# Kernel tuning notes

Hardware: AMD Instinct MI355X
Metric: run time of the kernel (lower is better)

## Reference

```python
import jax, jax.numpy as jnp
import numpy as np

NUM_HEADS = 16
HEAD_DIM = 64  # dim_qkv // num_heads


def setup_inputs() -> dict:
    key = jax.random.key(0)
    ks = jax.random.split(key, 6)
    B, N, D = 2, 2048, 1024
    s = 1.0 / np.sqrt(D)
    x = jax.random.normal(ks[0], (B, N, D), dtype=jnp.float32)
    Wq = jax.random.normal(ks[1], (D, D), dtype=jnp.float32) * s
    Wk = jax.random.normal(ks[2], (D, D), dtype=jnp.float32) * s
    Wv = jax.random.normal(ks[3], (D, D), dtype=jnp.float32) * s
    Wo = jax.random.normal(ks[4], (D, D), dtype=jnp.float32) * s
    z = jnp.zeros((D,), dtype=jnp.float32)
    return {"x": x, "Wq": Wq, "bq": z, "Wk": Wk, "bk": z,
            "Wv": Wv, "bv": z, "Wo": Wo, "bo": z}


def _split_heads(t):
    # [B, N, H*dh] -> [B, H, N, dh]
    B, N, _ = t.shape
    return t.reshape(B, N, NUM_HEADS, HEAD_DIM).transpose(0, 2, 1, 3)


def reference(x, Wq, bq, Wk, bk, Wv, bv, Wo, bo):
    q = _split_heads(x @ Wq + bq)
    k = _split_heads(x @ Wk + bk)
    v = _split_heads(x @ Wv + bv)
    scores = jnp.einsum('bhnd,bhmd->bhnm', q, k) / jnp.sqrt(
        jnp.asarray(HEAD_DIM, dtype=x.dtype))
    attn = jax.nn.softmax(scores, axis=-1)
    heads = jnp.einsum('bhnm,bhmd->bhnd', attn, v)  # [B, H, N, dh]
    B, H, N, dh = heads.shape
    merged = heads.transpose(0, 2, 1, 3).reshape(B, N, H * dh)
    # dropout is identity in deterministic/eval mode
    return merged @ Wo + bo
```

## Files before the change

### kernel.cpp

```cpp
#include <hip/hip_runtime.h>
#include <hip/hip_bf16.h>

typedef __bf16 bf16;
typedef __attribute__((ext_vector_type(8))) __bf16 bf16x8;
typedef __attribute__((ext_vector_type(4))) __bf16 bf16x4;
typedef __attribute__((ext_vector_type(4))) float f32x4;
typedef __attribute__((ext_vector_type(16))) float f32x16;
typedef unsigned int uint;

#define MFMA16(a, b, c) __builtin_amdgcn_mfma_f32_16x16x32_bf16(a, b, c, 0, 0, 0)
#define MFMA32(a, b, c) __builtin_amdgcn_mfma_f32_32x32x16_bf16(a, b, c, 0, 0, 0)

#define GLOAD_LDS(gp, lp) \
  __builtin_amdgcn_global_load_lds( \
      (const __attribute__((address_space(1))) void*)(gp), \
      (__attribute__((address_space(3))) void*)(lp), 16, 0, 0)

#define QSCALE 0.18033688011112042f

__device__ __forceinline__ uint pack2(float a, float b) {
  unsigned short x = __builtin_bit_cast(unsigned short, (bf16)a);
  unsigned short y = __builtin_bit_cast(unsigned short, (bf16)b);
  return (uint)x | ((uint)y << 16);
}

__global__ __launch_bounds__(256) void cvt_x_kernel(const float* __restrict__ x,
                                                    bf16* __restrict__ y) {
  int i = (blockIdx.x * 256 + threadIdx.x) * 8;
  float4 a = *(const float4*)(x + i);
  float4 b = *(const float4*)(x + i + 4);
  bf16x8 v;
  v[0] = (bf16)a.x; v[1] = (bf16)a.y; v[2] = (bf16)a.z; v[3] = (bf16)a.w;
  v[4] = (bf16)b.x; v[5] = (bf16)b.y; v[6] = (bf16)b.z; v[7] = (bf16)b.w;
  *(bf16x8*)(y + i) = v;
}

__global__ __launch_bounds__(256) void wtrans_kernel(
    const float* __restrict__ W0, const float* __restrict__ W1,
    const float* __restrict__ W2, const float* __restrict__ W3,
    bf16* __restrict__ T0, bf16* __restrict__ T1,
    bf16* __restrict__ T2, bf16* __restrict__ T3) {
  const float* W; bf16* T;
  switch (blockIdx.z) {
    case 0: W = W0; T = T0; break;
    case 1: W = W1; T = T1; break;
    case 2: W = W2; T = T2; break;
    default: W = W3; T = T3; break;
  }
  const float scl = (blockIdx.z == 0) ? QSCALE : 1.0f;
  __shared__ float tile[32][33];
  int tx = threadIdx.x & 31;
  int ty = threadIdx.x >> 5;
  int bx = blockIdx.x * 32, by = blockIdx.y * 32;
#pragma unroll
  for (int i = 0; i < 32; i += 8)
    tile[ty + i][tx] = W[(size_t)(by + ty + i) * 1024 + bx + tx];
  __syncthreads();
#pragma unroll
  for (int i = 0; i < 32; i += 8)
    T[(size_t)(bx + ty + i) * 1024 + by + tx] = (bf16)(tile[tx][ty + i] * scl);
}

template <int MODE>
__global__ __launch_bounds__(256, 2) void gemm_kernel(
    const bf16* __restrict__ A, const bf16* __restrict__ Bt,
    const float* __restrict__ b0, const float* __restrict__ b1,
    const float* __restrict__ b2, bf16* __restrict__ o0,
    bf16* __restrict__ o1, bf16* __restrict__ o2, float* __restrict__ of) {
  __shared__ bf16 As[128 * 64];
  __shared__ bf16 Bs[128 * 64];
  const int t = threadIdx.x;
  const int lane = t & 63, wid = t >> 6;
  const int wy = wid >> 1, wx = wid & 1;
  const int lr = lane & 15, lg = lane >> 4;
  const int bm = blockIdx.y, bn = blockIdx.x;
  const bf16* Arow = A + (size_t)bm * 128 * 1024;
  const bf16* Brow = Bt + (size_t)bn * 128 * 1024;
  f32x4 acc[4][4] = {};

  for (int k0 = 0; k0 < 1024; k0 += 64) {
    __syncthreads();
#pragma unroll
    for (int i = 0; i < 4; i++) {
      int off = i * 256 + t;
      int row = off >> 3, ch = off & 7;
      int gch = ch ^ (row & 7);
      GLOAD_LDS(Arow + (size_t)row * 1024 + k0 + gch * 8, As + off * 8);
    }
#pragma unroll
    for (int i = 0; i < 4; i++) {
      int off = i * 256 + t;
      int row = off >> 3, ch = off & 7;
      int gch = ch ^ (row & 7);
      GLOAD_LDS(Brow + (size_t)row * 1024 + k0 + gch * 8, Bs + off * 8);
    }
    __syncthreads();
#pragma unroll
    for (int kh = 0; kh < 2; kh++) {
      bf16x8 af[4], bfr[4];
#pragma unroll
      for (int i = 0; i < 4; i++) {
        int row = wy * 64 + i * 16 + lr;
        int c = kh * 4 + lg;
        af[i] = *(const bf16x8*)(As + row * 64 + ((c ^ (row & 7)) << 3));
      }
#pragma unroll
      for (int j = 0; j < 4; j++) {
        int row = wx * 64 + j * 16 + lr;
        int c = kh * 4 + lg;
        bfr[j] = *(const bf16x8*)(Bs + row * 64 + ((c ^ (row & 7)) << 3));
      }
#pragma unroll
      for (int i = 0; i < 4; i++)
#pragma unroll
        for (int j = 0; j < 4; j++)
          acc[i][j] = MFMA16(af[i], bfr[j], acc[i][j]);
    }
  }

  const int seg = (MODE == 0) ? (bn >> 3) : 0;
  const float* bias = (MODE == 1) ? b0 : (seg == 0 ? b0 : (seg == 1 ? b1 : b2));
  const float bscale = (MODE == 0 && seg == 0) ? QSCALE : 1.0f;

#pragma unroll
  for (int i = 0; i < 4; i++) {
    const int rowb = bm * 128 + wy * 64 + i * 16 + lg * 4;
#pragma unroll
    for (int j = 0; j < 4; j++) {
      const int np = bn * 128 + wx * 64 + j * 16 + lr;
      const int col = np & 1023;
      const float bv = bias[col] * bscale;
      if (MODE == 1) {
#pragma unroll
        for (int r = 0; r < 4; r++)
          of[(size_t)(rowb + r) * 1024 + np] = acc[i][j][r] + bv;
      } else {
        const int h = col >> 6, d = col & 63;
        const int bb = rowb >> 11, nn = rowb & 2047;
        if (seg == 2) {
          bf16x4 pk;
#pragma unroll
          for (int r = 0; r < 4; r++) pk[r] = (bf16)(acc[i][j][r] + bv);
          *(bf16x4*)(o2 + (((size_t)bb * 16 + h) * 64 + d) * 2048 + nn) = pk;
        } else {
          bf16* dst = (seg == 0) ? o0 : o1;
#pragma unroll
          for (int r = 0; r < 4; r++)
            dst[(((size_t)bb * 16 + h) * 2048 + nn + r) * 64 + d] =
                (bf16)(acc[i][j][r] + bv);
        }
      }
    }
  }
}

__global__ __launch_bounds__(256, 2) void attn_kernel(
    const bf16* __restrict__ Q, const bf16* __restrict__ K,
    const bf16* __restrict__ Vt, bf16* __restrict__ Mg) {
  __shared__ bf16 Kl[2][4096];
  __shared__ bf16 Vl[2][4096];
  const int t = threadIdx.x;
  const int lane = t & 63, w = t >> 6;
  const int l31 = lane & 31, hi = lane >> 5;
  const int bh = blockIdx.y;
  const int b = bh >> 4, h = bh & 15;
  const bf16* Qh = Q + (size_t)bh * 2048 * 64;
  const bf16* Kh = K + (size_t)bh * 2048 * 64;
  const bf16* Vh = Vt + (size_t)bh * 64 * 2048;
  const int q_row = blockIdx.x * 128 + w * 32 + l31;

  bf16x8 qf[4];
#pragma unroll
  for (int dblk = 0; dblk < 4; dblk++)
    qf[dblk] = *(const bf16x8*)(Qh + (size_t)q_row * 64 + dblk * 16 + hi * 8);

  f32x16 o0 = {}, o1 = {};
  float lrun = 0.f;

#define STAGE(kt_, buf_)                                                     \
  {                                                                          \
    _Pragma("unroll") for (int i = 0; i < 2; i++) {                          \
      int off = i * 256 + t;                                                 \
      int row = off >> 3, ch = off & 7;                                      \
      int gch = ch ^ (row & 7);                                              \
      GLOAD_LDS(Kh + (size_t)(kt_) * 4096 + row * 64 + gch * 8,              \
                &Kl[buf_][off * 8]);                                         \
      GLOAD_LDS(Vh + (size_t)row * 2048 + (kt_) * 64 + gch * 8,              \
                &Vl[buf_][off * 8]);                                         \
    }                                                                        \
  }

  STAGE(0, 0);
  __syncthreads();

  for (int kt = 0; kt < 32; kt++) {
    const int cur = kt & 1;
    if (kt < 31) STAGE(kt + 1, cur ^ 1);

    f32x16 s0 = {}, s1 = {};
#pragma unroll
    for (int dblk = 0; dblk < 4; dblk++) {
      int c = dblk * 2 + hi;
      bf16x8 kf0 = *(const bf16x8*)&Kl[cur][l31 * 64 + ((c ^ (l31 & 7)) << 3)];
      bf16x8 kf1 = *(const bf16x8*)&Kl[cur][(32 + l31) * 64 + ((c ^ (l31 & 7)) << 3)];
      s0 = MFMA32(kf0, qf[dblk], s0);
      s1 = MFMA32(kf1, qf[dblk], s1);
    }

    float rs = 0.f;
#pragma unroll
    for (int r = 0; r < 16; r++) {
      s0[r] = __builtin_amdgcn_exp2f(s0[r]);
      s1[r] = __builtin_amdgcn_exp2f(s1[r]);
      rs += s0[r] + s1[r];
    }
    rs += __shfl_xor(rs, 32);
    lrun += rs;

    uint prc[8], prd[8];
#pragma unroll
    for (int s = 0; s < 4; s++) {
      prc[s] = pack2(s0[4 * s + 0], s0[4 * s + 1]);
      prd[s] = pack2(s0[4 * s + 2], s0[4 * s + 3]);
      prc[4 + s] = pack2(s1[4 * s + 0], s1[4 * s + 1]);
      prd[4 + s] = pack2(s1[4 * s + 2], s1[4 * s + 3]);
    }

#pragma unroll
    for (int kb = 0; kb < 4; kb++) {
      const int sb = (kb >> 1) * 4 + (kb & 1) * 2;
      uint sendc = hi ? prc[sb] : prc[sb + 1];
      uint sendd = hi ? prd[sb] : prd[sb + 1];
      uint recvc = __shfl_xor(sendc, 32);
      uint recvd = __shfl_xor(sendd, 32);
      union { uint u[4]; bf16x8 v; } pf;
      pf.u[0] = hi ? recvc : prc[sb];
      pf.u[1] = hi ? recvd : prd[sb];
      pf.u[2] = hi ? prc[sb + 1] : recvc;
      pf.u[3] = hi ? prd[sb + 1] : recvd;

      int c = kb * 2 + hi;
      bf16x8 vt0 = *(const bf16x8*)&Vl[cur][l31 * 64 + ((c ^ (l31 & 7)) << 3)];
      bf16x8 vt1 = *(const bf16x8*)&Vl[cur][(32 + l31) * 64 + ((c ^ (l31 & 7)) << 3)];
      o0 = MFMA32(vt0, pf.v, o0);
      o1 = MFMA32(vt1, pf.v, o1);
    }

    __syncthreads();
  }

  const float inv = 1.f / lrun;
  bf16* orow = Mg + ((size_t)b * 2048 + q_row) * 1024 + h * 64;
#pragma unroll
  for (int s = 0; s < 4; s++) {
    bf16x4 p0, p1;
#pragma unroll
    for (int r = 0; r < 4; r++) {
      p0[r] = (bf16)(o0[4 * s + r] * inv);
      p1[r] = (bf16)(o1[4 * s + r] * inv);
    }
    *(bf16x4*)(orow + s * 8 + hi * 4) = p0;
    *(bf16x4*)(orow + 32 + s * 8 + hi * 4) = p1;
  }
}

extern "C" void kernel_launch(void* const* d_in, const int* in_sizes, int n_in,
                              void* d_out, int out_size, void* d_ws, size_t ws_size,
                              hipStream_t stream) {
  const float* x  = (const float*)d_in[0];
  const float* Wq = (const float*)d_in[1];
  const float* bq = (const float*)d_in[2];
  const float* Wk = (const float*)d_in[3];
  const float* bk = (const float*)d_in[4];
  const float* Wv = (const float*)d_in[5];
  const float* bv = (const float*)d_in[6];
  const float* Wo = (const float*)d_in[7];
  const float* bo = (const float*)d_in[8];
  float* out = (float*)d_out;
  char* ws = (char*)d_ws;
  const size_t MiB = 1u << 20;

  bf16* Xb    = (bf16*)(ws);
  bf16* Mg    = Xb;
  bf16* Wqkv  = (bf16*)(ws + 8 * MiB);
  bf16* WoT   = (bf16*)(ws + 14 * MiB);
  bf16* Qb    = (bf16*)(ws + 16 * MiB);
  bf16* Kb    = (bf16*)(ws + 24 * MiB);
  bf16* Vtb   = (bf16*)(ws + 32 * MiB);

  cvt_x_kernel<<<2048, 256, 0, stream>>>(x, Xb);
  wtrans_kernel<<<dim3(32, 32, 4), 256, 0, stream>>>(
      Wq, Wk, Wv, Wo, Wqkv, Wqkv + (1u << 20), Wqkv + (2u << 20), WoT);
  gemm_kernel<0><<<dim3(24, 32), 256, 0, stream>>>(
      Xb, Wqkv, bq, bk, bv, Qb, Kb, Vtb, nullptr);
  attn_kernel<<<dim3(16, 32), 256, 0, stream>>>(Qb, Kb, Vtb, Mg);
  gemm_kernel<1><<<dim3(8, 32), 256, 0, stream>>>(
      Mg, WoT, bo, nullptr, nullptr, nullptr, nullptr, nullptr, out);
  (void)in_sizes; (void)n_in; (void)out_size; (void)ws_size;
}
```

Before: 129.9 us.

## Merge prep kernels, XCD-aware block remap, larger attention K/V tiles, narrower output GEMM tiles

The x conversion and weight transpose kernels are merged into one launch, saving a kernel launch. The QKV GEMM, output GEMM and attention now remap block indices so that neighbouring tiles (or all query blocks of one head) land on the same XCD for L2 reuse. Attention stages 128-key tiles instead of 64, halving the loop iterations and barriers at the cost of doubled LDS use and more registers. The output projection becomes a dedicated kernel with 128x64 tiles, doubling the grid to improve CU occupancy.

```diff
diff --git a/kernel.cpp b/kernel.cpp
--- a/kernel.cpp
+++ b/kernel.cpp
@@ -24,34 +24,37 @@
   return (uint)x | ((uint)y << 16);
 }
 
-__global__ __launch_bounds__(256) void cvt_x_kernel(const float* __restrict__ x,
-                                                    bf16* __restrict__ y) {
-  int i = (blockIdx.x * 256 + threadIdx.x) * 8;
-  float4 a = *(const float4*)(x + i);
-  float4 b = *(const float4*)(x + i + 4);
-  bf16x8 v;
-  v[0] = (bf16)a.x; v[1] = (bf16)a.y; v[2] = (bf16)a.z; v[3] = (bf16)a.w;
-  v[4] = (bf16)b.x; v[5] = (bf16)b.y; v[6] = (bf16)b.z; v[7] = (bf16)b.w;
-  *(bf16x8*)(y + i) = v;
-}
-
-__global__ __launch_bounds__(256) void wtrans_kernel(
+__global__ __launch_bounds__(256) void prep_kernel(
+    const float* __restrict__ x, bf16* __restrict__ y,
     const float* __restrict__ W0, const float* __restrict__ W1,
     const float* __restrict__ W2, const float* __restrict__ W3,
     bf16* __restrict__ T0, bf16* __restrict__ T1,
     bf16* __restrict__ T2, bf16* __restrict__ T3) {
+  const int bid = blockIdx.x;
+  if (bid < 2048) {
+    int i = (bid * 256 + threadIdx.x) * 8;
+    float4 a = *(const float4*)(x + i);
+    float4 b = *(const float4*)(x + i + 4);
+    bf16x8 v;
+    v[0] = (bf16)a.x; v[1] = (bf16)a.y; v[2] = (bf16)a.z; v[3] = (bf16)a.w;
+    v[4] = (bf16)b.x; v[5] = (bf16)b.y; v[6] = (bf16)b.z; v[7] = (bf16)b.w;
+    *(bf16x8*)(y + i) = v;
+    return;
+  }
+  const int wq = bid - 2048;
+  const int z = wq >> 10, rem = wq & 1023;
   const float* W; bf16* T;
-  switch (blockIdx.z) {
+  switch (z) {
     case 0: W = W0; T = T0; break;
     case 1: W = W1; T = T1; break;
     case 2: W = W2; T = T2; break;
     default: W = W3; T = T3; break;
   }
-  const float scl = (blockIdx.z == 0) ? QSCALE : 1.0f;
+  const float scl = (z == 0) ? QSCALE : 1.0f;
   __shared__ float tile[32][33];
   int tx = threadIdx.x & 31;
   int ty = threadIdx.x >> 5;
-  int bx = blockIdx.x * 32, by = blockIdx.y * 32;
+  int bx = (rem & 31) * 32, by = (rem >> 5) * 32;
 #pragma unroll
   for (int i = 0; i < 32; i += 8)
     tile[ty + i][tx] = W[(size_t)(by + ty + i) * 1024 + bx + tx];
@@ -61,19 +64,20 @@
     T[(size_t)(bx + ty + i) * 1024 + by + tx] = (bf16)(tile[tx][ty + i] * scl);
 }
 
-template <int MODE>
-__global__ __launch_bounds__(256, 2) void gemm_kernel(
+__global__ __launch_bounds__(256, 2) void gemm_qkv_kernel(
     const bf16* __restrict__ A, const bf16* __restrict__ Bt,
     const float* __restrict__ b0, const float* __restrict__ b1,
     const float* __restrict__ b2, bf16* __restrict__ o0,
-    bf16* __restrict__ o1, bf16* __restrict__ o2, float* __restrict__ of) {
+    bf16* __restrict__ o1, bf16* __restrict__ o2) {
   __shared__ bf16 As[128 * 64];
   __shared__ bf16 Bs[128 * 64];
+  const int f = blockIdx.y * 24 + blockIdx.x;
+  const int wg = (f % 8) * 96 + f / 8;
+  const int bn = wg % 24, bm = wg / 24;
   const int t = threadIdx.x;
   const int lane = t & 63, wid = t >> 6;
   const int wy = wid >> 1, wx = wid & 1;
   const int lr = lane & 15, lg = lane >> 4;
-  const int bm = blockIdx.y, bn = blockIdx.x;
   const bf16* Arow = A + (size_t)bm * 128 * 1024;
   const bf16* Brow = Bt + (size_t)bn * 128 * 1024;
   f32x4 acc[4][4] = {};
@@ -118,9 +122,9 @@
     }
   }
 
-  const int seg = (MODE == 0) ? (bn >> 3) : 0;
-  const float* bias = (MODE == 1) ? b0 : (seg == 0 ? b0 : (seg == 1 ? b1 : b2));
-  const float bscale = (MODE == 0 && seg == 0) ? QSCALE : 1.0f;
+  const int seg = bn >> 3;
+  const float* bias = (seg == 0) ? b0 : (seg == 1 ? b1 : b2);
+  const float bscale = (seg == 0) ? QSCALE : 1.0f;
 
 #pragma unroll
   for (int i = 0; i < 4; i++) {
@@ -130,26 +134,90 @@
       const int np = bn * 128 + wx * 64 + j * 16 + lr;
       const int col = np & 1023;
       const float bv = bias[col] * bscale;
-      if (MODE == 1) {
+      const int h = col >> 6, d = col & 63;
+      const int bb = rowb >> 11, nn = rowb & 2047;
+      if (seg == 2) {
+        bf16x4 pk;
+#pragma unroll
+        for (int r = 0; r < 4; r++) pk[r] = (bf16)(acc[i][j][r] + bv);
+        *(bf16x4*)(o2 + (((size_t)bb * 16 + h) * 64 + d) * 2048 + nn) = pk;
+      } else {
+        bf16* dst = (seg == 0) ? o0 : o1;
 #pragma unroll
         for (int r = 0; r < 4; r++)
-          of[(size_t)(rowb + r) * 1024 + np] = acc[i][j][r] + bv;
-      } else {
-        const int h = col >> 6, d = col & 63;
-        const int bb = rowb >> 11, nn = rowb & 2047;
-        if (seg == 2) {
-          bf16x4 pk;
-#pragma unroll
-          for (int r = 0; r < 4; r++) pk[r] = (bf16)(acc[i][j][r] + bv);
-          *(bf16x4*)(o2 + (((size_t)bb * 16 + h) * 64 + d) * 2048 + nn) = pk;
-        } else {
-          bf16* dst = (seg == 0) ? o0 : o1;
-#pragma unroll
-          for (int r = 0; r < 4; r++)
-            dst[(((size_t)bb * 16 + h) * 2048 + nn + r) * 64 + d] =
-                (bf16)(acc[i][j][r] + bv);
-        }
-      }
+          dst[(((size_t)bb * 16 + h) * 2048 + nn + r) * 64 + d] =
+              (bf16)(acc[i][j][r] + bv);
+      }
+    }
+  }
+}
+
+__global__ __launch_bounds__(256, 2) void gemmo_kernel(
+    const bf16* __restrict__ A, const bf16* __restrict__ Bt,
+    const float* __restrict__ bias, float* __restrict__ out) {
+  __shared__ bf16 As[128 * 64];
+  __shared__ bf16 Bs[64 * 64];
+  const int f = blockIdx.y * 16 + blockIdx.x;
+  const int wg = (f & 7) * 64 + (f >> 3);
+  const int bn = wg & 15, bm = wg >> 4;
+  const int t = threadIdx.x;
+  const int lane = t & 63, wid = t >> 6;
+  const int wy = wid >> 1, wx = wid & 1;
+  const int lr = lane & 15, lg = lane >> 4;
+  const bf16* Arow = A + (size_t)bm * 128 * 1024;
+  const bf16* Brow = Bt + (size_t)bn * 64 * 1024;
+  f32x4 acc[4][2] = {};
+
+  for (int k0 = 0; k0 < 1024; k0 += 64) {
+    __syncthreads();
+#pragma unroll
+    for (int i = 0; i < 4; i++) {
+      int off = i * 256 + t;
+      int row = off >> 3, ch = off & 7;
+      int gch = ch ^ (row & 7);
+      GLOAD_LDS(Arow + (size_t)row * 1024 + k0 + gch * 8, As + off * 8);
+    }
+#pragma unroll
+    for (int i = 0; i < 2; i++) {
+      int off = i * 256 + t;
+      int row = off >> 3, ch = off & 7;
+      int gch = ch ^ (row & 7);
+      GLOAD_LDS(Brow + (size_t)row * 1024 + k0 + gch * 8, Bs + off * 8);
+    }
+    __syncthreads();
+#pragma unroll
+    for (int kh = 0; kh < 2; kh++) {
+      bf16x8 af[4], bfr[2];
+#pragma unroll
+      for (int i = 0; i < 4; i++) {
+        int row = wy * 64 + i * 16 + lr;
+        int c = kh * 4 + lg;
+        af[i] = *(const bf16x8*)(As + row * 64 + ((c ^ (row & 7)) << 3));
+      }
+#pragma unroll
+      for (int j = 0; j < 2; j++) {
+        int row = wx * 32 + j * 16 + lr;
+        int c = kh * 4 + lg;
+        bfr[j] = *(const bf16x8*)(Bs + row * 64 + ((c ^ (row & 7)) << 3));
+      }
+#pragma unroll
+      for (int i = 0; i < 4; i++)
+#pragma unroll
+        for (int j = 0; j < 2; j++)
+          acc[i][j] = MFMA16(af[i], bfr[j], acc[i][j]);
+    }
+  }
+
+#pragma unroll
+  for (int i = 0; i < 4; i++) {
+    const int rowb = bm * 128 + wy * 64 + i * 16 + lg * 4;
+#pragma unroll
+    for (int j = 0; j < 2; j++) {
+      const int col = bn * 64 + wx * 32 + j * 16 + lr;
+      const float bv = bias[col];
+#pragma unroll
+      for (int r = 0; r < 4; r++)
+        out[(size_t)(rowb + r) * 1024 + col] = acc[i][j][r] + bv;
     }
   }
 }
@@ -157,17 +225,20 @@
 __global__ __launch_bounds__(256, 2) void attn_kernel(
     const bf16* __restrict__ Q, const bf16* __restrict__ K,
     const bf16* __restrict__ Vt, bf16* __restrict__ Mg) {
-  __shared__ bf16 Kl[2][4096];
-  __shared__ bf16 Vl[2][4096];
+  __shared__ bf16 Kl[2][8192];
+  __shared__ bf16 Vl[2][8192];
   const int t = threadIdx.x;
   const int lane = t & 63, w = t >> 6;
   const int l31 = lane & 31, hi = lane >> 5;
-  const int bh = blockIdx.y;
+  const int f = blockIdx.y * 16 + blockIdx.x;
+  const int xcd = f & 7, slot = f >> 3;
+  const int bh = xcd * 4 + (slot >> 4);
+  const int bx = slot & 15;
   const int b = bh >> 4, h = bh & 15;
   const bf16* Qh = Q + (size_t)bh * 2048 * 64;
   const bf16* Kh = K + (size_t)bh * 2048 * 64;
   const bf16* Vh = Vt + (size_t)bh * 64 * 2048;
-  const int q_row = blockIdx.x * 128 + w * 32 + l31;
+  const int q_row = bx * 128 + w * 32 + l31;
 
   bf16x8 qf[4];
 #pragma unroll
@@ -177,57 +248,65 @@
   f32x16 o0 = {}, o1 = {};
   float lrun = 0.f;
 
-#define STAGE(kt_, buf_)                                                     \
-  {                                                                          \
-    _Pragma("unroll") for (int i = 0; i < 2; i++) {                          \
-      int off = i * 256 + t;                                                 \
-      int row = off >> 3, ch = off & 7;                                      \
-      int gch = ch ^ (row & 7);                                              \
-      GLOAD_LDS(Kh + (size_t)(kt_) * 4096 + row * 64 + gch * 8,              \
-                &Kl[buf_][off * 8]);                                         \
-      GLOAD_LDS(Vh + (size_t)row * 2048 + (kt_) * 64 + gch * 8,              \
-                &Vl[buf_][off * 8]);                                         \
-    }                                                                        \
+#define STAGE(kt_, buf_)                                                      \
+  {                                                                           \
+    _Pragma("unroll") for (int i = 0; i < 4; i++) {                           \
+      int off = i * 256 + t;                                                  \
+      int row = off >> 3, ch = off & 7;                                       \
+      int gch = ch ^ (row & 7);                                               \
+      GLOAD_LDS(Kh + (size_t)(kt_) * 8192 + row * 64 + gch * 8,               \
+                &Kl[buf_][off * 8]);                                          \
+    }                                                                         \
+    _Pragma("unroll") for (int i = 0; i < 4; i++) {                           \
+      int off = i * 256 + t;                                                  \
+      int row = off >> 4, ch = off & 15;                                      \
+      int gch = ch ^ (row & 15);                                              \
+      GLOAD_LDS(Vh + (size_t)row * 2048 + (kt_) * 128 + gch * 8,              \
+                &Vl[buf_][off * 8]);                                          \
+    }                                                                         \
   }
 
   STAGE(0, 0);
   __syncthreads();
 
-  for (int kt = 0; kt < 32; kt++) {
+  for (int kt = 0; kt < 16; kt++) {
     const int cur = kt & 1;
-    if (kt < 31) STAGE(kt + 1, cur ^ 1);
-
-    f32x16 s0 = {}, s1 = {};
+    if (kt < 15) STAGE(kt + 1, cur ^ 1);
+
+    f32x16 s[4] = {{0}, {0}, {0}, {0}};
 #pragma unroll
     for (int dblk = 0; dblk < 4; dblk++) {
-      int c = dblk * 2 + hi;
-      bf16x8 kf0 = *(const bf16x8*)&Kl[cur][l31 * 64 + ((c ^ (l31 & 7)) << 3)];
-      bf16x8 kf1 = *(const bf16x8*)&Kl[cur][(32 + l31) * 64 + ((c ^ (l31 & 7)) << 3)];
-      s0 = MFMA32(kf0, qf[dblk], s0);
-      s1 = MFMA32(kf1, qf[dblk], s1);
+      const int c = dblk * 2 + hi;
+#pragma unroll
+      for (int rg = 0; rg < 4; rg++) {
+        const int row = rg * 32 + l31;
+        bf16x8 kf = *(const bf16x8*)&Kl[cur][row * 64 + ((c ^ (row & 7)) << 3)];
+        s[rg] = MFMA32(kf, qf[dblk], s[rg]);
+      }
     }
 
     float rs = 0.f;
 #pragma unroll
-    for (int r = 0; r < 16; r++) {
-      s0[r] = __builtin_amdgcn_exp2f(s0[r]);
-      s1[r] = __builtin_amdgcn_exp2f(s1[r]);
-      rs += s0[r] + s1[r];
-    }
+    for (int rg = 0; rg < 4; rg++)
+#pragma unroll
+      for (int r = 0; r < 16; r++) {
+        s[rg][r] = __builtin_amdgcn_exp2f(s[rg][r]);
+        rs += s[rg][r];
+      }
     rs += __shfl_xor(rs, 32);
     lrun += rs;
 
-    uint prc[8], prd[8];
-#pragma unroll
-    for (int s = 0; s < 4; s++) {
-      prc[s] = pack2(s0[4 * s + 0], s0[4 * s + 1]);
-      prd[s] = pack2(s0[4 * s + 2], s0[4 * s + 3]);
-      prc[4 + s] = pack2(s1[4 * s + 0], s1[4 * s + 1]);
-      prd[4 + s] = pack2(s1[4 * s + 2], s1[4 * s + 3]);
-    }
-
-#pragma unroll
-    for (int kb = 0; kb < 4; kb++) {
+    uint prc[16], prd[16];
+#pragma unroll
+    for (int g = 0; g < 4; g++)
+#pragma unroll
+      for (int si = 0; si < 4; si++) {
+        prc[g * 4 + si] = pack2(s[g][4 * si + 0], s[g][4 * si + 1]);
+        prd[g * 4 + si] = pack2(s[g][4 * si + 2], s[g][4 * si + 3]);
+      }
+
+#pragma unroll
+    for (int kb = 0; kb < 8; kb++) {
       const int sb = (kb >> 1) * 4 + (kb & 1) * 2;
       uint sendc = hi ? prc[sb] : prc[sb + 1];
       uint sendd = hi ? prd[sb] : prd[sb + 1];
@@ -239,9 +318,10 @@
       pf.u[2] = hi ? prc[sb + 1] : recvc;
       pf.u[3] = hi ? prd[sb + 1] : recvd;
 
-      int c = kb * 2 + hi;
-      bf16x8 vt0 = *(const bf16x8*)&Vl[cur][l31 * 64 + ((c ^ (l31 & 7)) << 3)];
-      bf16x8 vt1 = *(const bf16x8*)&Vl[cur][(32 + l31) * 64 + ((c ^ (l31 & 7)) << 3)];
+      const int c = kb * 2 + hi;
+      bf16x8 vt0 = *(const bf16x8*)&Vl[cur][l31 * 128 + ((c ^ (l31 & 15)) << 3)];
+      bf16x8 vt1 =
+          *(const bf16x8*)&Vl[cur][(32 + l31) * 128 + ((c ^ ((32 + l31) & 15)) << 3)];
       o0 = MFMA32(vt0, pf.v, o0);
       o1 = MFMA32(vt1, pf.v, o1);
     }
@@ -252,15 +332,15 @@
   const float inv = 1.f / lrun;
   bf16* orow = Mg + ((size_t)b * 2048 + q_row) * 1024 + h * 64;
 #pragma unroll
-  for (int s = 0; s < 4; s++) {
+  for (int si = 0; si < 4; si++) {
     bf16x4 p0, p1;
 #pragma unroll
     for (int r = 0; r < 4; r++) {
-      p0[r] = (bf16)(o0[4 * s + r] * inv);
-      p1[r] = (bf16)(o1[4 * s + r] * inv);
-    }
-    *(bf16x4*)(orow + s * 8 + hi * 4) = p0;
-    *(bf16x4*)(orow + 32 + s * 8 + hi * 4) = p1;
+      p0[r] = (bf16)(o0[4 * si + r] * inv);
+      p1[r] = (bf16)(o1[4 * si + r] * inv);
+    }
+    *(bf16x4*)(orow + si * 8 + hi * 4) = p0;
+    *(bf16x4*)(orow + 32 + si * 8 + hi * 4) = p1;
   }
 }
 
@@ -280,21 +360,19 @@
   char* ws = (char*)d_ws;
   const size_t MiB = 1u << 20;
 
-  bf16* Xb    = (bf16*)(ws);
-  bf16* Mg    = Xb;
-  bf16* Wqkv  = (bf16*)(ws + 8 * MiB);
-  bf16* WoT   = (bf16*)(ws + 14 * MiB);
-  bf16* Qb    = (bf16*)(ws + 16 * MiB);
-  bf16* Kb    = (bf16*)(ws + 24 * MiB);
-  bf16* Vtb   = (bf16*)(ws + 32 * MiB);
-
-  cvt_x_kernel<<<2048, 256, 0, stream>>>(x, Xb);
-  wtrans_kernel<<<dim3(32, 32, 4), 256, 0, stream>>>(
-      Wq, Wk, Wv, Wo, Wqkv, Wqkv + (1u << 20), Wqkv + (2u << 20), WoT);
-  gemm_kernel<0><<<dim3(24, 32), 256, 0, stream>>>(
-      Xb, Wqkv, bq, bk, bv, Qb, Kb, Vtb, nullptr);
+  bf16* Xb   = (bf16*)(ws);
+  bf16* Mg   = Xb;
+  bf16* Wqkv = (bf16*)(ws + 8 * MiB);
+  bf16* WoT  = (bf16*)(ws + 14 * MiB);
+  bf16* Qb   = (bf16*)(ws + 16 * MiB);
+  bf16* Kb   = (bf16*)(ws + 24 * MiB);
+  bf16* Vtb  = (bf16*)(ws + 32 * MiB);
+
+  prep_kernel<<<6144, 256, 0, stream>>>(
+      x, Xb, Wq, Wk, Wv, Wo, Wqkv, Wqkv + (1u << 20), Wqkv + (2u << 20), WoT);
+  gemm_qkv_kernel<<<dim3(24, 32), 256, 0, stream>>>(
+      Xb, Wqkv, bq, bk, bv, Qb, Kb, Vtb);
   attn_kernel<<<dim3(16, 32), 256, 0, stream>>>(Qb, Kb, Vtb, Mg);
-  gemm_kernel<1><<<dim3(8, 32), 256, 0, stream>>>(
-      Mg, WoT, bo, nullptr, nullptr, nullptr, nullptr, nullptr, out);
+  gemmo_kernel<<<dim3(16, 32), 256, 0, stream>>>(Mg, WoT, bo, out);
   (void)in_sizes; (void)n_in; (void)out_size; (void)ws_size;
 }
```

Result: faster. 113.3 us (-12.8%).
